# Kernel optimization log

Measured on AMD Instinct MI355X. Metric: run time of the kernel, lower is better.

The kernel has to match this reference:

```python
import jax, jax.numpy as jnp
import numpy as np

N_POINTS = 131072  # 32 clouds * 4096 points
N_SEG = 32


def setup_inputs() -> dict:
    key = jax.random.key(0)
    ks = jax.random.split(key, 8)
    x = jax.random.normal(ks[0], (N_POINTS, 256), dtype=jnp.float32)
    pos = jax.random.normal(ks[1], (N_POINTS, 3), dtype=jnp.float32)
    # sorted segment ids, every segment non-empty (equal-size clouds)
    batch = jnp.repeat(jnp.arange(N_SEG, dtype=jnp.int32), N_POINTS // N_SEG)
    def lin(k, fan_in, fan_out):
        s = 1.0 / np.sqrt(fan_in)
        return jax.random.uniform(k, (fan_in, fan_out), jnp.float32, -s, s)
    W1 = lin(ks[2], 259, 256); b1 = jnp.zeros((256,), jnp.float32)
    W2 = lin(ks[3], 256, 512); b2 = jnp.zeros((512,), jnp.float32)
    W3 = lin(ks[4], 512, 1024); b3 = jnp.zeros((1024,), jnp.float32)
    return {"x": x, "pos": pos, "batch": batch,
            "W1": W1, "b1": b1, "W2": W2, "b2": b2, "W3": W3, "b3": b3}


def reference(x, pos, batch, W1, b1, W2, b2, W3, b3):
    # concat point features with coordinates: [N, 256+3]
    h = jnp.concatenate([x, pos], axis=1)
    # shared point-wise MLP (Linear + ReLU per layer)
    h = jax.nn.relu(h @ W1 + b1)   # [N, 256]
    h = jax.nn.relu(h @ W2 + b2)   # [N, 512]
    h = jax.nn.relu(h @ W3 + b3)   # [N, 1024]
    # global_max_pool: batch-indexed segment max -> [N_SEG, 1024]
    return jax.ops.segment_max(h, batch, num_segments=N_SEG)
```

## Files before the change

### kernel.cpp

```cpp
#include <hip/hip_runtime.h>
#include <stdint.h>

typedef unsigned short ushort_t;
typedef short shortx8 __attribute__((ext_vector_type(8)));
typedef float floatx4 __attribute__((ext_vector_type(4)));
typedef unsigned short ushortx8 __attribute__((ext_vector_type(8)));

__device__ __forceinline__ unsigned short f2bf(float f) {
  union { float f; unsigned int u; } v; v.f = f;
  unsigned int u = v.u;
  return (unsigned short)((u + 0x7fffu + ((u >> 16) & 1u)) >> 16);
}

__device__ __forceinline__ void gload_lds16(const void* g, void* l) {
  __builtin_amdgcn_global_load_lds(
      (const __attribute__((address_space(1))) unsigned int*)g,
      (__attribute__((address_space(3))) unsigned int*)l, 16, 0, 0);
}

__global__ void prep_w_k(const float* __restrict__ W1, const float* __restrict__ W2,
                         const float* __restrict__ W3, ushort_t* __restrict__ W1T,
                         ushort_t* __restrict__ W2T, ushort_t* __restrict__ W3T) {
  int idx = blockIdx.x * blockDim.x + threadIdx.x;
  const float* in; ushort_t* out; int K, N;
  if (idx < 256 * 256)                  { in = W1; out = W1T; K = 256; N = 256; }
  else if (idx < 256 * 256 + 512 * 256) { idx -= 256 * 256; in = W2; out = W2T; K = 256; N = 512; }
  else if (idx < 256 * 256 + 512 * 256 + 1024 * 512) {
    idx -= 256 * 256 + 512 * 256; in = W3; out = W3T; K = 512; N = 1024;
  } else return;
  int n = idx / K, k = idx - n * K;
  out[idx] = f2bf(in[k * N + n]);
}

template <int K, int NOUT, int MODE>
__global__ __launch_bounds__(256, 2) void gemm_kernel(
    const ushort_t* __restrict__ A, const ushort_t* __restrict__ BT,
    const float* __restrict__ bias, ushort_t* __restrict__ C,
    const float* __restrict__ pos, const float* __restrict__ W1tail,
    float* __restrict__ pool, const float* __restrict__ Afp) {
  __shared__ __align__(16) ushort_t As[128 * 64];
  __shared__ __align__(16) ushort_t Bs[128 * 64];

  const int m0 = blockIdx.x * 128;
  const int n0 = blockIdx.y * 128;
  const int tid = threadIdx.x;
  const int w = tid >> 6;
  const int l = tid & 63;
  const int wm = w >> 1, wn = w & 1;
  const int lane16 = l & 15, lq = l >> 4;
  const int s7 = lane16 & 7;

  const int srow = l >> 3;
  const int sg = (l & 7) ^ srow;

  floatx4 acc[4][4] = {};

  for (int k0 = 0; k0 < K; k0 += 64) {
    if (MODE == 1) {
#pragma unroll
      for (int rep = 0; rep < 4; ++rep) {
        const int g = rep * 256 + tid;
        const int row = g >> 3, slot = g & 7;
        const int sgr = slot ^ (row & 7);
        const float4* src = (const float4*)(Afp + (size_t)(m0 + row) * K + k0 + sgr * 8);
        float4 a = src[0], b = src[1];
        ushortx8 v;
        v[0] = f2bf(a.x); v[1] = f2bf(a.y); v[2] = f2bf(a.z); v[3] = f2bf(a.w);
        v[4] = f2bf(b.x); v[5] = f2bf(b.y); v[6] = f2bf(b.z); v[7] = f2bf(b.w);
        *(ushortx8*)(As + row * 64 + slot * 8) = v;
      }
    } else {
#pragma unroll
      for (int r = 0; r < 4; ++r) {
        const int c = r * 4 + w;
        const int row = c * 8 + srow;
        gload_lds16(A + (size_t)(m0 + row) * K + k0 + sg * 8, As + c * 512);
      }
    }
#pragma unroll
    for (int r = 0; r < 4; ++r) {
      const int c = r * 4 + w;
      const int row = c * 8 + srow;
      gload_lds16(BT + (size_t)(n0 + row) * K + k0 + sg * 8, Bs + c * 512);
    }
    __syncthreads();
#pragma unroll
    for (int kk = 0; kk < 2; ++kk) {
      shortx8 af[4], bfr[4];
#pragma unroll
      for (int i = 0; i < 4; ++i) {
        const int row = wm * 64 + i * 16 + lane16;
        af[i] = *(const shortx8*)(As + row * 64 + ((kk * 4 + lq) ^ s7) * 8);
      }
#pragma unroll
      for (int j = 0; j < 4; ++j) {
        const int row = wn * 64 + j * 16 + lane16;
        bfr[j] = *(const shortx8*)(Bs + row * 64 + ((kk * 4 + lq) ^ s7) * 8);
      }
#pragma unroll
      for (int i = 0; i < 4; ++i)
#pragma unroll
        for (int j = 0; j < 4; ++j)
          acc[i][j] = __builtin_amdgcn_mfma_f32_16x16x32_bf16(af[i], bfr[j], acc[i][j], 0, 0, 0);
    }
    __syncthreads();
  }

  float bv[4];
#pragma unroll
  for (int j = 0; j < 4; ++j) bv[j] = bias[n0 + wn * 64 + j * 16 + lane16];

  if (MODE == 2) {
    const int seg = m0 >> 12;
#pragma unroll
    for (int j = 0; j < 4; ++j) {
      float vmax = 0.0f;
#pragma unroll
      for (int i = 0; i < 4; ++i)
#pragma unroll
        for (int r = 0; r < 4; ++r) vmax = fmaxf(vmax, acc[i][j][r] + bv[j]);
      vmax = fmaxf(vmax, __shfl_xor(vmax, 16, 64));
      vmax = fmaxf(vmax, __shfl_xor(vmax, 32, 64));
      if (l < 16) {
        int n = n0 + wn * 64 + j * 16 + lane16;
        atomicMax((int*)(pool + (size_t)seg * NOUT + n), __float_as_int(vmax));
      }
    }
  } else {
#pragma unroll
    for (int i = 0; i < 4; ++i) {
#pragma unroll
      for (int r = 0; r < 4; ++r) {
        int m = m0 + wm * 64 + i * 16 + lq * 4 + r;
        float p0 = 0.f, p1 = 0.f, p2 = 0.f;
        if (MODE == 1) { p0 = pos[m * 3 + 0]; p1 = pos[m * 3 + 1]; p2 = pos[m * 3 + 2]; }
#pragma unroll
        for (int j = 0; j < 4; ++j) {
          int n = n0 + wn * 64 + j * 16 + lane16;
          float v = acc[i][j][r] + bv[j];
          if (MODE == 1) v += p0 * W1tail[n] + p1 * W1tail[256 + n] + p2 * W1tail[512 + n];
          v = fmaxf(v, 0.0f);
          C[(size_t)m * NOUT + n] = f2bf(v);
        }
      }
    }
  }
}


extern "C" void kernel_launch(void* const* d_in, const int* in_sizes, int n_in,
                              void* d_out, int out_size, void* d_ws, size_t ws_size,
                              hipStream_t stream) {
  const float* x   = (const float*)d_in[0];
  const float* pos = (const float*)d_in[1];
  const float* W1 = (const float*)d_in[3];
  const float* b1 = (const float*)d_in[4];
  const float* W2 = (const float*)d_in[5];
  const float* b2 = (const float*)d_in[6];
  const float* W3 = (const float*)d_in[7];
  const float* b3 = (const float*)d_in[8];
  float* out = (float*)d_out;

  const int M = in_sizes[0] / 256;

  char* ws = (char*)d_ws;
  ushort_t* H2  = (ushort_t*)ws;
  ushort_t* H1  = (ushort_t*)(ws + (size_t)M * 512 * 2);
  ushort_t* W1T = (ushort_t*)(ws + (size_t)M * 512 * 2 + (size_t)M * 256 * 2);
  ushort_t* W2T = W1T + 256 * 256;
  ushort_t* W3T = W2T + 512 * 256;

  const int ntr = 256 * 256 + 512 * 256 + 1024 * 512;
  prep_w_k<<<(ntr + 255) / 256, 256, 0, stream>>>(W1, W2, W3, W1T, W2T, W3T);

  gemm_kernel<256, 256, 1><<<dim3(M / 128, 2), 256, 0, stream>>>(
      nullptr, W1T, b1, H1, pos, W1 + 256 * 256, nullptr, x);
  gemm_kernel<256, 512, 0><<<dim3(M / 128, 4), 256, 0, stream>>>(
      H1, W2T, b2, H2, nullptr, nullptr, nullptr, nullptr);
  gemm_kernel<512, 1024, 2><<<dim3(M / 128, 8), 256, 0, stream>>>(
      H2, W3T, b3, nullptr, nullptr, nullptr, out, nullptr);
}
```

Baseline: 451.2 us.

## Add 256x256 double-buffered pipelined GEMM for layers 2 and 3 with block swizzle

Adds a new 512-thread GEMM kernel with 256x256 tiles, double-buffered LDS, and interleaved global-to-LDS staging, LDS reads and MFMA phases, using explicit waitcnt, barriers and setprio. Layers 2 and 3 now use it, and all GEMM kernels remap block indices with an XCD-style swizzle. The aim is to overlap memory loads with MFMA work and to get more reuse from larger tiles. In exchange it uses a lot of LDS (128KB) and many registers, which limits occupancy, and the hand-tuned wait counts are fragile.

```diff
diff --git a/kernel.cpp b/kernel.cpp
--- a/kernel.cpp
+++ b/kernel.cpp
@@ -41,8 +41,12 @@
   __shared__ __align__(16) ushort_t As[128 * 64];
   __shared__ __align__(16) ushort_t Bs[128 * 64];
 
-  const int m0 = blockIdx.x * 128;
-  const int n0 = blockIdx.y * 128;
+  constexpr int GY = NOUT / 128;
+  const int wlin = blockIdx.x + blockIdx.y * gridDim.x;
+  const int nwg = gridDim.x * GY;
+  const int swz = (wlin & 7) * (nwg >> 3) + (wlin >> 3);
+  const int m0 = (swz / GY) * 128;
+  const int n0 = (swz % GY) * 128;
   const int tid = threadIdx.x;
   const int w = tid >> 6;
   const int l = tid & 63;
@@ -144,6 +148,219 @@
         }
       }
     }
+  }
+}
+
+template <int K, int NOUT, int MODE>
+__global__ __launch_bounds__(512, 2) void gemm256_kernel(
+    const ushort_t* __restrict__ A, const ushort_t* __restrict__ BT,
+    const float* __restrict__ bias, ushort_t* __restrict__ C,
+    float* __restrict__ pool) {
+  __shared__ __align__(16) ushort_t As[2][256 * 64];
+  __shared__ __align__(16) ushort_t Bs[2][256 * 64];
+
+  constexpr int GY = NOUT / 256;
+  constexpr int T = K / 64;
+
+  const int wlin = blockIdx.x + blockIdx.y * gridDim.x;
+  const int nwg = gridDim.x * GY;
+  const int swz = (wlin & 7) * (nwg >> 3) + (wlin >> 3);
+  const int m0 = (swz / GY) * 256;
+  const int n0 = (swz % GY) * 256;
+
+  const int tid = threadIdx.x;
+  const int w8 = tid >> 6;
+  const int l = tid & 63;
+  const int wm = w8 >> 2, wn = w8 & 3;
+  const int lane16 = l & 15, lq = l >> 4;
+  const int s7 = lane16 & 7;
+
+  const int sgl = (l & 7) ^ (l >> 3);
+  const int lrow = l >> 3;
+  const int arow0 = w8 << 3;
+  const int brow0 = ((w8 >> 1) << 6) + ((w8 & 1) << 3);
+
+  floatx4 acc[2][4][4] = {};
+  shortx8 af[4][2];
+  shortx8 bfr[4][2];
+
+#define STAGEA(bb, tt, h, rb)                                                  \
+  do {                                                                         \
+    const int base_ = (h)*64 + (rb)*128 + arow0;                               \
+    gload_lds16(A + (size_t)(m0 + base_ + lrow) * K + (tt)*64 + sgl * 8,       \
+                &As[bb][base_ * 64]);                                          \
+  } while (0)
+#define STAGEB(bb, tt, h, rb)                                                  \
+  do {                                                                         \
+    const int base_ = brow0 + (h)*32 + (rb)*16;                                \
+    gload_lds16(BT + (size_t)(n0 + base_ + lrow) * K + (tt)*64 + sgl * 8,      \
+                &Bs[bb][base_ * 64]);                                          \
+  } while (0)
+#define READA(bb, mh)                                                          \
+  {                                                                            \
+    _Pragma("unroll") for (int i = 0; i < 4; ++i) {                            \
+      const int row_ = wm * 128 + (mh)*64 + i * 16 + lane16;                   \
+      _Pragma("unroll") for (int ks = 0; ks < 2; ++ks) {                       \
+        const int sl_ = ((ks << 2) | lq) ^ s7;                                 \
+        af[i][ks] = *(const shortx8*)(&As[bb][row_ * 64 + sl_ * 8]);           \
+      }                                                                        \
+    }                                                                          \
+  }
+#define READB(bb, jh)                                                          \
+  {                                                                            \
+    _Pragma("unroll") for (int jj = 0; jj < 2; ++jj) {                         \
+      const int j_ = (jh)*2 + jj;                                              \
+      const int row_ = wn * 64 + j_ * 16 + lane16;                             \
+      _Pragma("unroll") for (int ks = 0; ks < 2; ++ks) {                       \
+        const int sl_ = ((ks << 2) | lq) ^ s7;                                 \
+        bfr[j_][ks] = *(const shortx8*)(&Bs[bb][row_ * 64 + sl_ * 8]);         \
+      }                                                                        \
+    }                                                                          \
+  }
+#define DOMFMA(mh, jh)                                                         \
+  {                                                                            \
+    _Pragma("unroll") for (int ks = 0; ks < 2; ++ks)                           \
+    _Pragma("unroll") for (int i = 0; i < 4; ++i)                              \
+    _Pragma("unroll") for (int jj = 0; jj < 2; ++jj)                           \
+      acc[mh][i][(jh)*2 + jj] = __builtin_amdgcn_mfma_f32_16x16x32_bf16(       \
+          af[i][ks], bfr[(jh)*2 + jj][ks], acc[mh][i][(jh)*2 + jj], 0, 0, 0);  \
+  }
+#define WAITV(n)                                                               \
+  do {                                                                         \
+    asm volatile("s_waitcnt vmcnt(" #n ")" ::: "memory");                      \
+    __builtin_amdgcn_sched_barrier(0);                                         \
+  } while (0)
+#define WAITL()                                                                \
+  do {                                                                         \
+    asm volatile("s_waitcnt lgkmcnt(0)" ::: "memory");                         \
+    __builtin_amdgcn_sched_barrier(0);                                         \
+  } while (0)
+#define BAR()                                                                  \
+  do {                                                                         \
+    __builtin_amdgcn_sched_barrier(0);                                         \
+    asm volatile("" ::: "memory");                                             \
+    __builtin_amdgcn_s_barrier();                                              \
+    asm volatile("" ::: "memory");                                             \
+    __builtin_amdgcn_sched_barrier(0);                                         \
+  } while (0)
+
+  STAGEA(0, 0, 0, 0); STAGEA(0, 0, 0, 1);
+  STAGEB(0, 0, 0, 0); STAGEB(0, 0, 0, 1);
+  STAGEB(0, 0, 1, 0); STAGEB(0, 0, 1, 1);
+  STAGEA(0, 0, 1, 0); STAGEA(0, 0, 1, 1);
+
+  for (int t = 0; t < T - 1; ++t) {
+    const int buf = t & 1;
+    const int nbuf = buf ^ 1;
+    WAITV(4);
+    BAR();
+    READA(buf, 0);
+    READB(buf, 0);
+    STAGEA(nbuf, t + 1, 0, 0); STAGEA(nbuf, t + 1, 0, 1);
+    BAR();
+    WAITL();
+    __builtin_amdgcn_s_setprio(1);
+    DOMFMA(0, 0);
+    __builtin_amdgcn_s_setprio(0);
+    WAITV(4);
+    BAR();
+    READB(buf, 1);
+    STAGEB(nbuf, t + 1, 0, 0); STAGEB(nbuf, t + 1, 0, 1);
+    BAR();
+    WAITL();
+    __builtin_amdgcn_s_setprio(1);
+    DOMFMA(0, 1);
+    __builtin_amdgcn_s_setprio(0);
+    WAITV(4);
+    BAR();
+    READA(buf, 1);
+    STAGEB(nbuf, t + 1, 1, 0); STAGEB(nbuf, t + 1, 1, 1);
+    BAR();
+    WAITL();
+    __builtin_amdgcn_s_setprio(1);
+    DOMFMA(1, 0);
+    __builtin_amdgcn_s_setprio(0);
+    STAGEA(nbuf, t + 1, 1, 0); STAGEA(nbuf, t + 1, 1, 1);
+    BAR();
+    __builtin_amdgcn_s_setprio(1);
+    DOMFMA(1, 1);
+    __builtin_amdgcn_s_setprio(0);
+  }
+  {
+    const int buf = (T - 1) & 1;
+    WAITV(4);
+    BAR();
+    READA(buf, 0);
+    READB(buf, 0);
+    BAR();
+    WAITL();
+    __builtin_amdgcn_s_setprio(1);
+    DOMFMA(0, 0);
+    __builtin_amdgcn_s_setprio(0);
+    WAITV(2);
+    BAR();
+    READB(buf, 1);
+    BAR();
+    WAITL();
+    __builtin_amdgcn_s_setprio(1);
+    DOMFMA(0, 1);
+    __builtin_amdgcn_s_setprio(0);
+    WAITV(0);
+    BAR();
+    READA(buf, 1);
+    BAR();
+    WAITL();
+    __builtin_amdgcn_s_setprio(1);
+    DOMFMA(1, 0);
+    DOMFMA(1, 1);
+    __builtin_amdgcn_s_setprio(0);
+  }
+#undef STAGEA
+#undef STAGEB
+#undef READA
+#undef READB
+#undef DOMFMA
+#undef WAITV
+#undef WAITL
+#undef BAR
+
+  float bv[4];
+#pragma unroll
+  for (int j = 0; j < 4; ++j) bv[j] = bias[n0 + wn * 64 + j * 16 + lane16];
+
+  if (MODE == 2) {
+    const int seg = m0 >> 12;
+#pragma unroll
+    for (int j = 0; j < 4; ++j) {
+      float mp = acc[0][0][j][0];
+#pragma unroll
+      for (int mh = 0; mh < 2; ++mh)
+#pragma unroll
+        for (int i = 0; i < 4; ++i)
+#pragma unroll
+          for (int r = 0; r < 4; ++r) mp = fmaxf(mp, acc[mh][i][j][r]);
+      float vmax = fmaxf(mp + bv[j], 0.0f);
+      vmax = fmaxf(vmax, __shfl_xor(vmax, 16, 64));
+      vmax = fmaxf(vmax, __shfl_xor(vmax, 32, 64));
+      if (l < 16) {
+        const int n = n0 + wn * 64 + j * 16 + lane16;
+        atomicMax((int*)(pool + (size_t)seg * NOUT + n), __float_as_int(vmax));
+      }
+    }
+  } else {
+#pragma unroll
+    for (int mh = 0; mh < 2; ++mh)
+#pragma unroll
+      for (int i = 0; i < 4; ++i)
+#pragma unroll
+        for (int r = 0; r < 4; ++r) {
+          const int m = m0 + wm * 128 + mh * 64 + i * 16 + lq * 4 + r;
+#pragma unroll
+          for (int j = 0; j < 4; ++j) {
+            const int n = n0 + wn * 64 + j * 16 + lane16;
+            C[(size_t)m * NOUT + n] = f2bf(fmaxf(acc[mh][i][j][r] + bv[j], 0.0f));
+          }
+        }
   }
 }
 
@@ -175,8 +392,8 @@
 
   gemm_kernel<256, 256, 1><<<dim3(M / 128, 2), 256, 0, stream>>>(
       nullptr, W1T, b1, H1, pos, W1 + 256 * 256, nullptr, x);
-  gemm_kernel<256, 512, 0><<<dim3(M / 128, 4), 256, 0, stream>>>(
-      H1, W2T, b2, H2, nullptr, nullptr, nullptr, nullptr);
-  gemm_kernel<512, 1024, 2><<<dim3(M / 128, 8), 256, 0, stream>>>(
-      H2, W3T, b3, nullptr, nullptr, nullptr, out, nullptr);
-}
+  gemm256_kernel<256, 512, 0><<<dim3(M / 256, 2), 512, 0, stream>>>(
+      H1, W2T, b2, H2, nullptr);
+  gemm256_kernel<512, 1024, 2><<<dim3(M / 256, 4), 512, 0, stream>>>(
+      H2, W3T, b3, nullptr, out);
+}
```

New measurement: 405.9 us. 10.0% less time.

## Add double-buffered 256x256 MFMA32 GEMM kernel for layers two and three

Applied to the files above, without the earlier changes.

Adds a 512-thread GEMM kernel with 256x256 tiles and double-buffered LDS staging via global_load_lds, using 32x32x16 bf16 MFMAs with explicit waitcnt, sched barriers and setprio. It is used for the second and third layers, and a workgroup-index swizzle is applied to both kernels for cache locality. The aim is to raise arithmetic intensity and overlap global loads with MFMA work, at the cost of 128KB of LDS per block and possible occupancy or register limits. The fused segment-max epilogue is adapted to the 32x32 accumulator layout.

```diff
diff --git a/kernel.cpp b/kernel.cpp
--- a/kernel.cpp
+++ b/kernel.cpp
@@ -4,6 +4,7 @@
 typedef unsigned short ushort_t;
 typedef short shortx8 __attribute__((ext_vector_type(8)));
 typedef float floatx4 __attribute__((ext_vector_type(4)));
+typedef float floatx16 __attribute__((ext_vector_type(16)));
 typedef unsigned short ushortx8 __attribute__((ext_vector_type(8)));
 
 __device__ __forceinline__ unsigned short f2bf(float f) {
@@ -41,8 +42,12 @@
   __shared__ __align__(16) ushort_t As[128 * 64];
   __shared__ __align__(16) ushort_t Bs[128 * 64];
 
-  const int m0 = blockIdx.x * 128;
-  const int n0 = blockIdx.y * 128;
+  constexpr int GY = NOUT / 128;
+  const int wlin = blockIdx.x + blockIdx.y * gridDim.x;
+  const int nwg = gridDim.x * GY;
+  const int swz = (wlin & 7) * (nwg >> 3) + (wlin >> 3);
+  const int m0 = (swz / GY) * 128;
+  const int n0 = (swz % GY) * 128;
   const int tid = threadIdx.x;
   const int w = tid >> 6;
   const int l = tid & 63;
@@ -110,40 +115,189 @@
 #pragma unroll
   for (int j = 0; j < 4; ++j) bv[j] = bias[n0 + wn * 64 + j * 16 + lane16];
 
+#pragma unroll
+  for (int i = 0; i < 4; ++i) {
+#pragma unroll
+    for (int r = 0; r < 4; ++r) {
+      int m = m0 + wm * 64 + i * 16 + lq * 4 + r;
+      float p0 = 0.f, p1 = 0.f, p2 = 0.f;
+      if (MODE == 1) { p0 = pos[m * 3 + 0]; p1 = pos[m * 3 + 1]; p2 = pos[m * 3 + 2]; }
+#pragma unroll
+      for (int j = 0; j < 4; ++j) {
+        int n = n0 + wn * 64 + j * 16 + lane16;
+        float v = acc[i][j][r] + bv[j];
+        if (MODE == 1) v += p0 * W1tail[n] + p1 * W1tail[256 + n] + p2 * W1tail[512 + n];
+        v = fmaxf(v, 0.0f);
+        C[(size_t)m * NOUT + n] = f2bf(v);
+      }
+    }
+  }
+}
+
+template <int K, int NOUT, int MODE>
+__global__ __launch_bounds__(512, 2) void gemm256_kernel(
+    const ushort_t* __restrict__ A, const ushort_t* __restrict__ BT,
+    const float* __restrict__ bias, ushort_t* __restrict__ C,
+    float* __restrict__ pool) {
+  __shared__ __align__(16) ushort_t As[2][256 * 64];
+  __shared__ __align__(16) ushort_t Bs[2][256 * 64];
+
+  constexpr int GY = NOUT / 256;
+  constexpr int T = K / 64;
+
+  const int wlin = blockIdx.x + blockIdx.y * gridDim.x;
+  const int nwg = gridDim.x * GY;
+  const int swz = (wlin & 7) * (nwg >> 3) + (wlin >> 3);
+  const int m0 = (swz / GY) * 256;
+  const int n0 = (swz % GY) * 256;
+
+  const int tid = threadIdx.x;
+  const int w8 = tid >> 6;
+  const int l = tid & 63;
+  const int wm = w8 >> 2, wn = w8 & 3;
+  const int l31 = l & 31, lk = l >> 5;
+  const int s7 = l & 7;
+
+  const int sgl = (l & 7) ^ (l >> 3);
+  const int lrow = l >> 3;
+  const int arow0 = w8 << 3;
+  const int brow0 = ((w8 >> 1) << 6) + ((w8 & 1) << 3);
+
+  floatx16 acc[4][2] = {};
+  shortx8 a_[2][4];
+  shortx8 b_[2][4];
+
+#define STAGEA(bb, tt, h, rb)                                                  \
+  do {                                                                         \
+    const int base_ = (h)*64 + (rb)*128 + arow0;                               \
+    gload_lds16(A + (size_t)(m0 + base_ + lrow) * K + (tt)*64 + sgl * 8,       \
+                &As[bb][base_ * 64]);                                          \
+  } while (0)
+#define STAGEB(bb, tt, h, rb)                                                  \
+  do {                                                                         \
+    const int base_ = brow0 + (h)*32 + (rb)*16;                                \
+    gload_lds16(BT + (size_t)(n0 + base_ + lrow) * K + (tt)*64 + sgl * 8,      \
+                &Bs[bb][base_ * 64]);                                          \
+  } while (0)
+#define STAGE_ALL(bb, tt)                                                      \
+  do {                                                                         \
+    STAGEA(bb, tt, 0, 0); STAGEA(bb, tt, 0, 1);                                \
+    STAGEA(bb, tt, 1, 0); STAGEA(bb, tt, 1, 1);                                \
+    STAGEB(bb, tt, 0, 0); STAGEB(bb, tt, 0, 1);                                \
+    STAGEB(bb, tt, 1, 0); STAGEB(bb, tt, 1, 1);                                \
+  } while (0)
+#define RDA(bb, mh, i, ks)                                                     \
+  a_[i][ks] = *(const shortx8*)(&As[bb][(wm * 128 + (mh)*64 + (i)*32 + l31) * 64 + \
+                                        ((((ks) << 1) | lk) ^ s7) * 8])
+#define RDB(bb, nt, ks)                                                        \
+  b_[nt][ks] = *(const shortx8*)(&Bs[bb][(wn * 64 + (nt)*32 + l31) * 64 +      \
+                                         ((((ks) << 1) | lk) ^ s7) * 8])
+#define DOMFMA4(mh, ks)                                                        \
+  do {                                                                         \
+    acc[(mh)*2 + 0][0] = __builtin_amdgcn_mfma_f32_32x32x16_bf16(              \
+        a_[0][ks], b_[0][ks], acc[(mh)*2 + 0][0], 0, 0, 0);                    \
+    acc[(mh)*2 + 0][1] = __builtin_amdgcn_mfma_f32_32x32x16_bf16(              \
+        a_[0][ks], b_[1][ks], acc[(mh)*2 + 0][1], 0, 0, 0);                    \
+    acc[(mh)*2 + 1][0] = __builtin_amdgcn_mfma_f32_32x32x16_bf16(              \
+        a_[1][ks], b_[0][ks], acc[(mh)*2 + 1][0], 0, 0, 0);                    \
+    acc[(mh)*2 + 1][1] = __builtin_amdgcn_mfma_f32_32x32x16_bf16(              \
+        a_[1][ks], b_[1][ks], acc[(mh)*2 + 1][1], 0, 0, 0);                    \
+  } while (0)
+#define WAITV(n)                                                               \
+  do {                                                                         \
+    asm volatile("s_waitcnt vmcnt(" #n ")" ::: "memory");                      \
+    __builtin_amdgcn_sched_barrier(0);                                         \
+  } while (0)
+#define WAITL(n)                                                               \
+  do {                                                                         \
+    asm volatile("s_waitcnt lgkmcnt(" #n ")" ::: "memory");                    \
+    __builtin_amdgcn_sched_barrier(0);                                         \
+  } while (0)
+#define BAR()                                                                  \
+  do {                                                                         \
+    __builtin_amdgcn_sched_barrier(0);                                         \
+    asm volatile("" ::: "memory");                                             \
+    __builtin_amdgcn_s_barrier();                                              \
+    asm volatile("" ::: "memory");                                             \
+    __builtin_amdgcn_sched_barrier(0);                                         \
+  } while (0)
+
+  STAGE_ALL(0, 0);
+
+  for (int t = 0; t < T; ++t) {
+    const int buf = t & 1;
+    BAR();
+    if (t + 1 < T) {
+      STAGE_ALL(buf ^ 1, t + 1);
+      WAITV(8);
+    } else {
+      WAITV(0);
+    }
+#pragma unroll
+    for (int ks = 0; ks < 4; ++ks) {
+      RDA(buf, 0, 0, ks); RDA(buf, 0, 1, ks);
+      RDB(buf, 0, ks);    RDB(buf, 1, ks);
+      __builtin_amdgcn_sched_barrier(0);
+    }
+    __builtin_amdgcn_s_setprio(1);
+    WAITL(12); DOMFMA4(0, 0);
+    WAITL(8);  DOMFMA4(0, 1);
+    WAITL(4);  DOMFMA4(0, 2);
+    WAITL(0);  DOMFMA4(0, 3);
+    __builtin_amdgcn_s_setprio(0);
+#pragma unroll
+    for (int ks = 0; ks < 4; ++ks) {
+      RDA(buf, 1, 0, ks); RDA(buf, 1, 1, ks);
+      __builtin_amdgcn_sched_barrier(0);
+    }
+    __builtin_amdgcn_s_setprio(1);
+    WAITL(6); DOMFMA4(1, 0);
+    WAITL(4); DOMFMA4(1, 1);
+    WAITL(2); DOMFMA4(1, 2);
+    WAITL(0); DOMFMA4(1, 3);
+    __builtin_amdgcn_s_setprio(0);
+  }
+#undef STAGEA
+#undef STAGEB
+#undef STAGE_ALL
+#undef RDA
+#undef RDB
+#undef DOMFMA4
+#undef WAITV
+#undef WAITL
+#undef BAR
+
+  float bv[2];
+#pragma unroll
+  for (int nt = 0; nt < 2; ++nt) bv[nt] = bias[n0 + wn * 64 + nt * 32 + l31];
+
   if (MODE == 2) {
     const int seg = m0 >> 12;
 #pragma unroll
-    for (int j = 0; j < 4; ++j) {
-      float vmax = 0.0f;
-#pragma unroll
-      for (int i = 0; i < 4; ++i)
-#pragma unroll
-        for (int r = 0; r < 4; ++r) vmax = fmaxf(vmax, acc[i][j][r] + bv[j]);
-      vmax = fmaxf(vmax, __shfl_xor(vmax, 16, 64));
+    for (int nt = 0; nt < 2; ++nt) {
+      float mp = acc[0][nt][0];
+#pragma unroll
+      for (int mi = 0; mi < 4; ++mi)
+#pragma unroll
+        for (int r = 0; r < 16; ++r) mp = fmaxf(mp, acc[mi][nt][r]);
+      float vmax = fmaxf(mp + bv[nt], 0.0f);
       vmax = fmaxf(vmax, __shfl_xor(vmax, 32, 64));
-      if (l < 16) {
-        int n = n0 + wn * 64 + j * 16 + lane16;
+      if (l < 32) {
+        const int n = n0 + wn * 64 + nt * 32 + l31;
         atomicMax((int*)(pool + (size_t)seg * NOUT + n), __float_as_int(vmax));
       }
     }
   } else {
 #pragma unroll
-    for (int i = 0; i < 4; ++i) {
-#pragma unroll
-      for (int r = 0; r < 4; ++r) {
-        int m = m0 + wm * 64 + i * 16 + lq * 4 + r;
-        float p0 = 0.f, p1 = 0.f, p2 = 0.f;
-        if (MODE == 1) { p0 = pos[m * 3 + 0]; p1 = pos[m * 3 + 1]; p2 = pos[m * 3 + 2]; }
-#pragma unroll
-        for (int j = 0; j < 4; ++j) {
-          int n = n0 + wn * 64 + j * 16 + lane16;
-          float v = acc[i][j][r] + bv[j];
-          if (MODE == 1) v += p0 * W1tail[n] + p1 * W1tail[256 + n] + p2 * W1tail[512 + n];
-          v = fmaxf(v, 0.0f);
-          C[(size_t)m * NOUT + n] = f2bf(v);
+    for (int mi = 0; mi < 4; ++mi)
+#pragma unroll
+      for (int nt = 0; nt < 2; ++nt)
+#pragma unroll
+        for (int r = 0; r < 16; ++r) {
+          const int m = m0 + wm * 128 + mi * 32 + (r & 3) + 8 * (r >> 2) + 4 * lk;
+          const int n = n0 + wn * 64 + nt * 32 + l31;
+          C[(size_t)m * NOUT + n] = f2bf(fmaxf(acc[mi][nt][r] + bv[nt], 0.0f));
         }
-      }
-    }
   }
 }
 
@@ -175,8 +329,8 @@
 
   gemm_kernel<256, 256, 1><<<dim3(M / 128, 2), 256, 0, stream>>>(
       nullptr, W1T, b1, H1, pos, W1 + 256 * 256, nullptr, x);
-  gemm_kernel<256, 512, 0><<<dim3(M / 128, 4), 256, 0, stream>>>(
-      H1, W2T, b2, H2, nullptr, nullptr, nullptr, nullptr);
-  gemm_kernel<512, 1024, 2><<<dim3(M / 128, 8), 256, 0, stream>>>(
-      H2, W3T, b3, nullptr, nullptr, nullptr, out, nullptr);
-}
+  gemm256_kernel<256, 512, 0><<<dim3(M / 256, 2), 512, 0, stream>>>(
+      H1, W2T, b2, H2, nullptr);
+  gemm256_kernel<512, 1024, 2><<<dim3(M / 256, 4), 512, 0, stream>>>(
+      H2, W3T, b3, nullptr, out);
+}
```

Result: faster. 429.1 us (-4.9%).
